# Optimization experiments

Hardware: AMD Instinct MI355X
Metric: run time of the kernel (lower is better)

## Reference

```python
import jax, jax.numpy as jnp
import numpy as np

D_K = 64

def setup_inputs() -> dict:
    key = jax.random.key(0)
    kq, kk, kv, km = jax.random.split(key, 4)
    B, H, S, D = 8, 8, 1024, D_K
    Q = jax.random.normal(kq, (B, H, S, D), dtype=jnp.float32)
    K = jax.random.normal(kk, (B, H, S, D), dtype=jnp.float32)
    V = jax.random.normal(kv, (B, H, S, D), dtype=jnp.float32)
    attention_masks = (jax.random.uniform(km, (B, 1, 1, S)) > 0.1).astype(jnp.float32)
    return {"Q": Q, "K": K, "V": V, "attention_masks": attention_masks}

def reference(Q, K, V, attention_masks):
    # scores = exp(QK^T / sqrt(d_k))  -- raw exp, NO max-subtraction (faithful to source)
    scale = 1.0 / np.sqrt(D_K).astype(np.float32)
    scores = jnp.exp(jnp.einsum('bhqd,bhkd->bhqk', Q, K) * scale)
    scores = scores * attention_masks  # multiplicative masking
    attention_scores = scores / (jnp.sum(scores, axis=-1, keepdims=True) + 1e-8)
    context = jnp.einsum('bhqk,bhkd->bhqd', attention_scores, V)
    return (context, attention_scores)
```

## Files before the change

kernel.cpp:

```cpp
#include <hip/hip_runtime.h>


typedef float    f32x4 __attribute__((ext_vector_type(4)));
typedef _Float16 f16x8 __attribute__((ext_vector_type(8)));
typedef _Float16 f16x4 __attribute__((ext_vector_type(4)));

#define MFMA32(A, B, C) __builtin_amdgcn_mfma_f32_16x16x32_f16((A), (B), (C), 0, 0, 0)
#define MFMA16(A, B, C) __builtin_amdgcn_mfma_f32_16x16x16f16((A), (B), (C), 0, 0, 0)

#define BHN 64
#define SEQ 1024
#define DIM 64

__device__ inline f16x8 cvt8(f32x4 a, f32x4 b) {
    f16x8 r;
    r[0] = (_Float16)a[0]; r[1] = (_Float16)a[1]; r[2] = (_Float16)a[2]; r[3] = (_Float16)a[3];
    r[4] = (_Float16)b[0]; r[5] = (_Float16)b[1]; r[6] = (_Float16)b[2]; r[7] = (_Float16)b[3];
    return r;
}

__global__ __launch_bounds__(256)
void cvt_kv(const float* __restrict__ K, const float* __restrict__ V,
            _Float16* __restrict__ Kh, _Float16* __restrict__ VTP)
{
    __shared__ _Float16 tile[128 * 65];
    const int bh = blockIdx.x >> 3;
    const int kc = blockIdx.x & 7;
    const int t  = threadIdx.x;
    const size_t base = ((size_t)bh * SEQ + (size_t)kc * 128) * DIM;

    for (int it = 0; it < 8; ++it) {
        int idx = it * 256 + t;
        int key = idx >> 4;
        int c4  = idx & 15;
        f32x4 kv = *(const f32x4*)(K + base + key * DIM + c4 * 4);
        f32x4 vv = *(const f32x4*)(V + base + key * DIM + c4 * 4);
        f16x4 kh4;
        kh4[0] = (_Float16)kv[0]; kh4[1] = (_Float16)kv[1];
        kh4[2] = (_Float16)kv[2]; kh4[3] = (_Float16)kv[3];
        *(f16x4*)(Kh + base + key * DIM + c4 * 4) = kh4;
        tile[key * 65 + c4 * 4 + 0] = (_Float16)vv[0];
        tile[key * 65 + c4 * 4 + 1] = (_Float16)vv[1];
        tile[key * 65 + c4 * 4 + 2] = (_Float16)vv[2];
        tile[key * 65 + c4 * 4 + 3] = (_Float16)vv[3];
    }
    __syncthreads();
    for (int it = 0; it < 8; ++it) {
        int flat = it * 256 + t;
        int ktl  = flat >> 8;
        int rem  = flat & 255;
        int l    = rem >> 2;
        int c    = rem & 3;
        f16x4 o;
        #pragma unroll
        for (int j = 0; j < 4; ++j)
            o[j] = tile[(ktl * 16 + ((l >> 4) << 2) + j) * 65 + c * 16 + (l & 15)];
        *(f16x4*)(VTP + (((size_t)bh * 64 + kc * 8 + ktl) * 64 + l) * 16 + c * 4) = o;
    }
}

template <bool PRECONV>
__global__ __launch_bounds__(256, 2)
void attn_main(const float* __restrict__ Q, const float* __restrict__ K,
               const float* __restrict__ V, const float* __restrict__ mask,
               const _Float16* __restrict__ Kh, const _Float16* __restrict__ VTP,
               float* __restrict__ ctx, float* __restrict__ scores)
{
    __shared__ _Float16 Et[32 * 1024];
    __shared__ float rs[4][2][16];

    const int bid = blockIdx.x;
    const int wg  = ((bid & 7) << 8) | (bid >> 3);
    const int bh  = wg >> 5;
    const int qb  = wg & 31;
    const int b   = bh >> 3;
    const int w    = threadIdx.x >> 6;
    const int lane = threadIdx.x & 63;
    const int col  = lane & 15;
    const int g    = lane >> 4;
    const int q0   = qb * 32;
    const int kb   = w * 256;
    const float scale = 0.125f;
    char* EtB = (char*)Et;

    f16x8 qf[2][2];
    {
        const float* qbase = Q + ((size_t)bh * SEQ + q0) * DIM;
        #pragma unroll
        for (int s = 0; s < 2; ++s)
            #pragma unroll
            for (int f = 0; f < 2; ++f) {
                const float* p = qbase + (s * 16 + col) * DIM + f * 32 + g * 8;
                qf[s][f] = cvt8(*(const f32x4*)p, *(const f32x4*)(p + 4));
            }
    }
    const float* mb = mask + (size_t)b * SEQ + kb;
    const _Float16* kbase = Kh + ((size_t)bh * SEQ + kb + col) * DIM + g * 8;
    const _Float16* vtpb  = VTP + (((size_t)bh * 64 + w * 16) * 64 + lane) * 16;

    f32x4 cacc[2][4];
    #pragma unroll
    for (int s = 0; s < 2; ++s)
        #pragma unroll
        for (int dt = 0; dt < 4; ++dt) cacc[s][dt] = (f32x4){0.f, 0.f, 0.f, 0.f};
    float rsum[2] = {0.f, 0.f};

    auto loadS = [&](int kt, f16x8& a, f16x8& c, f16x8& x, f16x8& y, f32x4& m) {
        if (PRECONV) {
            a = *(const f16x8*)(kbase + (size_t)kt * 16 * DIM);
            c = *(const f16x8*)(kbase + (size_t)kt * 16 * DIM + 32);
            x = *(const f16x8*)(vtpb + (size_t)kt * 64 * 16);
            y = *(const f16x8*)(vtpb + (size_t)kt * 64 * 16 + 8);
        } else {
            const float* kp = K + ((size_t)bh * SEQ + kb + kt * 16 + col) * DIM + g * 8;
            a = cvt8(*(const f32x4*)kp,        *(const f32x4*)(kp + 4));
            c = cvt8(*(const f32x4*)(kp + 32), *(const f32x4*)(kp + 36));
            #pragma unroll
            for (int e = 0; e < 8; ++e) {
                x[e] = (_Float16)V[((size_t)bh * SEQ + kb + kt * 16 + g * 4 + (e & 3)) * DIM + (e >> 2) * 16 + col];
                y[e] = (_Float16)V[((size_t)bh * SEQ + kb + kt * 16 + g * 4 + (e & 3)) * DIM + (2 + (e >> 2)) * 16 + col];
            }
        }
        m = *(const f32x4*)(mb + kt * 16 + g * 4);
    };

    auto body = [&](int kt, f16x8 k0, f16x8 k1, f16x8 va, f16x8 vb, f32x4 m4) {
        f16x4 pf[2];
        #pragma unroll
        for (int s = 0; s < 2; ++s) {
            f32x4 acc = {0.f, 0.f, 0.f, 0.f};
            acc = MFMA32(k0, qf[s][0], acc);
            acc = MFMA32(k1, qf[s][1], acc);
            const float e0 = __expf(acc[0] * scale) * m4[0];
            const float e1 = __expf(acc[1] * scale) * m4[1];
            const float e2 = __expf(acc[2] * scale) * m4[2];
            const float e3 = __expf(acc[3] * scale) * m4[3];
            rsum[s] += e0 + e1 + e2 + e3;
            f16x4 eh;
            eh[0] = (_Float16)e0; eh[1] = (_Float16)e1;
            eh[2] = (_Float16)e2; eh[3] = (_Float16)e3;
            pf[s] = eh;
            const int row = s * 16 + col;
            const int kg  = (w * 64 + kt * 4 + g) ^ ((row & 3) << 2);
            *(f16x4*)(EtB + row * 2048 + kg * 8) = eh;
        }
        f16x4 vt0 = __builtin_shufflevector(va, va, 0, 1, 2, 3);
        f16x4 vt1 = __builtin_shufflevector(va, va, 4, 5, 6, 7);
        f16x4 vt2 = __builtin_shufflevector(vb, vb, 0, 1, 2, 3);
        f16x4 vt3 = __builtin_shufflevector(vb, vb, 4, 5, 6, 7);
        cacc[0][0] = MFMA16(vt0, pf[0], cacc[0][0]);
        cacc[1][0] = MFMA16(vt0, pf[1], cacc[1][0]);
        cacc[0][1] = MFMA16(vt1, pf[0], cacc[0][1]);
        cacc[1][1] = MFMA16(vt1, pf[1], cacc[1][1]);
        cacc[0][2] = MFMA16(vt2, pf[0], cacc[0][2]);
        cacc[1][2] = MFMA16(vt2, pf[1], cacc[1][2]);
        cacc[0][3] = MFMA16(vt3, pf[0], cacc[0][3]);
        cacc[1][3] = MFMA16(vt3, pf[1], cacc[1][3]);
    };

    f16x8 k0A, k1A, vaA, vbA, k0B, k1B, vaB, vbB;
    f32x4 m4A, m4B;
    loadS(0, k0A, k1A, vaA, vbA, m4A);
    loadS(1, k0B, k1B, vaB, vbB, m4B);

    #pragma unroll 1
    for (int kt = 0; kt < 16; kt += 2) {
        f16x8 n0, n1, nx, ny;
        f32x4 nm;
        loadS((kt + 2) & 15, n0, n1, nx, ny, nm);
        body(kt, k0A, k1A, vaA, vbA, m4A);
        k0A = n0; k1A = n1; vaA = nx; vbA = ny; m4A = nm;

        loadS((kt + 3) & 15, n0, n1, nx, ny, nm);
        body(kt + 1, k0B, k1B, vaB, vbB, m4B);
        k0B = n0; k1B = n1; vaB = nx; vbB = ny; m4B = nm;
    }

    #pragma unroll
    for (int s = 0; s < 2; ++s) {
        float r = rsum[s];
        r += __shfl_xor(r, 16, 64);
        r += __shfl_xor(r, 32, 64);
        rsum[s] = r;
    }
    if (g == 0) {
        rs[w][0][col] = rsum[0];
        rs[w][1][col] = rsum[1];
    }
    __syncthreads();

    const int r0 = w * 8;
    float* srow = scores + ((size_t)bh * SEQ + q0) * SEQ;
    for (int j = 0; j < 8; ++j) {
        const int r  = r0 + j;
        const int si = r >> 4, ci = r & 15;
        const float invr = 1.0f / (rs[0][si][ci] + rs[1][si][ci] + rs[2][si][ci] + rs[3][si][ci] + 1e-8f);
        f16x4 ev[4];
        #pragma unroll
        for (int q = 0; q < 4; ++q) {
            const int kg = (q * 64 + lane) ^ ((r & 3) << 2);
            ev[q] = *(const f16x4*)(EtB + r * 2048 + kg * 8);
        }
        float* dst = srow + (size_t)r * SEQ + lane * 4;
        #pragma unroll
        for (int q = 0; q < 4; ++q) {
            f32x4 o;
            o[0] = (float)ev[q][0] * invr;
            o[1] = (float)ev[q][1] * invr;
            o[2] = (float)ev[q][2] * invr;
            o[3] = (float)ev[q][3] * invr;
            __builtin_nontemporal_store(o, (f32x4*)(dst + q * 256));
        }
    }

    __syncthreads();

    float* dumpf = (float*)Et;
    if (w != 0) {
        float* d = dumpf + (w - 1) * 2048;
        #pragma unroll
        for (int s = 0; s < 2; ++s)
            #pragma unroll
            for (int dt = 0; dt < 4; ++dt)
                #pragma unroll
                for (int i = 0; i < 4; ++i)
                    d[((s * 4 + dt) * 4 + i) * 64 + lane] = cacc[s][dt][i];
    }
    __syncthreads();
    if (w == 0) {
        #pragma unroll
        for (int s = 0; s < 2; ++s) {
            const float invs = 1.0f / (rs[0][s][col] + rs[1][s][col] + rs[2][s][col] + rs[3][s][col] + 1e-8f);
            #pragma unroll
            for (int dt = 0; dt < 4; ++dt) {
                f32x4 r = cacc[s][dt];
                #pragma unroll
                for (int ww = 0; ww < 3; ++ww) {
                    const float* d = dumpf + ww * 2048;
                    #pragma unroll
                    for (int i = 0; i < 4; ++i)
                        r[i] += d[((s * 4 + dt) * 4 + i) * 64 + lane];
                }
                r[0] *= invs; r[1] *= invs; r[2] *= invs; r[3] *= invs;
                *(f32x4*)(ctx + ((size_t)bh * SEQ + q0 + s * 16 + col) * DIM + dt * 16 + g * 4) = r;
            }
        }
    }
}

extern "C" void kernel_launch(void* const* d_in, const int* in_sizes, int n_in,
                              void* d_out, int out_size, void* d_ws, size_t ws_size,
                              hipStream_t stream)
{
    const float* Q    = (const float*)d_in[0];
    const float* K    = (const float*)d_in[1];
    const float* V    = (const float*)d_in[2];
    const float* mask = (const float*)d_in[3];
    float* ctx    = (float*)d_out;
    float* scores = ctx + (size_t)BHN * SEQ * DIM;

    const size_t elems = (size_t)BHN * SEQ * DIM;
    const size_t need  = elems * 2 * sizeof(_Float16);
    if (ws_size >= need) {
        _Float16* Kh  = (_Float16*)d_ws;
        _Float16* VTP = Kh + elems;
        cvt_kv<<<512, 256, 0, stream>>>(K, V, Kh, VTP);
        attn_main<true><<<2048, 256, 0, stream>>>(Q, K, V, mask, Kh, VTP, ctx, scores);
    } else {
        attn_main<false><<<2048, 256, 0, stream>>>(Q, K, V, mask, nullptr, nullptr, ctx, scores);
    }
}
```

Measured before the change: 93.83 us.

## Split attention into rowsum pass and streamed normalized score/PV pass

Adds a separate kernel that computes QK^T exponentials only to get per-row inverse sums. The main kernel then recomputes the scores already normalized and streams them to global memory in small double-buffered shared-memory chunks interleaved with the loop, instead of holding a full 32x1024 tile and writing it after a barrier. The intent is to overlap the large scores write with compute and cut shared-memory footprint. The cost is a second QK^T plus exp pass and an extra launch. The fallback path writes invp into the workspace without checking its size.

```diff
diff --git a/kernel.cpp b/kernel.cpp
--- a/kernel.cpp
+++ b/kernel.cpp
@@ -60,14 +60,90 @@
 }
 
 template <bool PRECONV>
+__global__ __launch_bounds__(256, 4)
+void rowsum_k(const float* __restrict__ Q, const float* __restrict__ K,
+              const float* __restrict__ mask, const _Float16* __restrict__ Kh,
+              float* __restrict__ invp)
+{
+    __shared__ float rs[4][4][16];
+    const int bid = blockIdx.x;
+    const int wg  = ((bid & 7) << 7) | (bid >> 3);
+    const int bh  = wg >> 4;
+    const int qb  = wg & 15;
+    const int b   = bh >> 3;
+    const int w    = threadIdx.x >> 6;
+    const int lane = threadIdx.x & 63;
+    const int col  = lane & 15;
+    const int g    = lane >> 4;
+    const int q0   = qb * 64;
+    const int kb   = w * 256;
+    const float scale = 0.125f;
+
+    f16x8 qf[4][2];
+    {
+        const float* qbase = Q + ((size_t)bh * SEQ + q0) * DIM;
+        #pragma unroll
+        for (int s = 0; s < 4; ++s)
+            #pragma unroll
+            for (int f = 0; f < 2; ++f) {
+                const float* p = qbase + (s * 16 + col) * DIM + f * 32 + g * 8;
+                qf[s][f] = cvt8(*(const f32x4*)p, *(const f32x4*)(p + 4));
+            }
+    }
+    const float* mb = mask + (size_t)b * SEQ + kb;
+
+    float rsum[4] = {0.f, 0.f, 0.f, 0.f};
+    #pragma unroll 1
+    for (int kt = 0; kt < 16; ++kt) {
+        f16x8 kf0, kf1;
+        if (PRECONV) {
+            const _Float16* kp = Kh + ((size_t)bh * SEQ + kb + kt * 16 + col) * DIM + g * 8;
+            kf0 = *(const f16x8*)kp;
+            kf1 = *(const f16x8*)(kp + 32);
+        } else {
+            const float* kp = K + ((size_t)bh * SEQ + kb + kt * 16 + col) * DIM + g * 8;
+            kf0 = cvt8(*(const f32x4*)kp,        *(const f32x4*)(kp + 4));
+            kf1 = cvt8(*(const f32x4*)(kp + 32), *(const f32x4*)(kp + 36));
+        }
+        f32x4 m4 = *(const f32x4*)(mb + kt * 16 + g * 4);
+        #pragma unroll
+        for (int s = 0; s < 4; ++s) {
+            f32x4 acc = {0.f, 0.f, 0.f, 0.f};
+            acc = MFMA32(kf0, qf[s][0], acc);
+            acc = MFMA32(kf1, qf[s][1], acc);
+            rsum[s] += __expf(acc[0] * scale) * m4[0] + __expf(acc[1] * scale) * m4[1]
+                     + __expf(acc[2] * scale) * m4[2] + __expf(acc[3] * scale) * m4[3];
+        }
+    }
+    #pragma unroll
+    for (int s = 0; s < 4; ++s) {
+        float r = rsum[s];
+        r += __shfl_xor(r, 16, 64);
+        r += __shfl_xor(r, 32, 64);
+        rsum[s] = r;
+    }
+    if (g == 0) {
+        #pragma unroll
+        for (int s = 0; s < 4; ++s) rs[w][s][col] = rsum[s];
+    }
+    __syncthreads();
+    if (w == 0) {
+        const int r = lane;
+        const float t = rs[0][r >> 4][r & 15] + rs[1][r >> 4][r & 15]
+                      + rs[2][r >> 4][r & 15] + rs[3][r >> 4][r & 15];
+        invp[(size_t)bh * SEQ + q0 + r] = 1.0f / (t + 1e-8f);
+    }
+}
+
+template <bool PRECONV>
 __global__ __launch_bounds__(256, 2)
-void attn_main(const float* __restrict__ Q, const float* __restrict__ K,
+void scorepv_k(const float* __restrict__ Q, const float* __restrict__ K,
                const float* __restrict__ V, const float* __restrict__ mask,
                const _Float16* __restrict__ Kh, const _Float16* __restrict__ VTP,
+               const float* __restrict__ invp,
                float* __restrict__ ctx, float* __restrict__ scores)
 {
-    __shared__ _Float16 Et[32 * 1024];
-    __shared__ float rs[4][2][16];
+    __shared__ _Float16 EC[4 * 2 * 32 * 64];
 
     const int bid = blockIdx.x;
     const int wg  = ((bid & 7) << 8) | (bid >> 3);
@@ -81,7 +157,7 @@
     const int q0   = qb * 32;
     const int kb   = w * 256;
     const float scale = 0.125f;
-    char* EtB = (char*)Et;
+    char* ECw = (char*)EC + w * 8192;
 
     f16x8 qf[2][2];
     {
@@ -94,16 +170,20 @@
                 qf[s][f] = cvt8(*(const f32x4*)p, *(const f32x4*)(p + 4));
             }
     }
+    float inv[2];
+    inv[0] = invp[(size_t)bh * SEQ + q0 + col];
+    inv[1] = invp[(size_t)bh * SEQ + q0 + 16 + col];
+
     const float* mb = mask + (size_t)b * SEQ + kb;
     const _Float16* kbase = Kh + ((size_t)bh * SEQ + kb + col) * DIM + g * 8;
     const _Float16* vtpb  = VTP + (((size_t)bh * 64 + w * 16) * 64 + lane) * 16;
+    float* srow = scores + ((size_t)bh * SEQ + q0) * SEQ + kb;
 
     f32x4 cacc[2][4];
     #pragma unroll
     for (int s = 0; s < 2; ++s)
         #pragma unroll
         for (int dt = 0; dt < 4; ++dt) cacc[s][dt] = (f32x4){0.f, 0.f, 0.f, 0.f};
-    float rsum[2] = {0.f, 0.f};
 
     auto loadS = [&](int kt, f16x8& a, f16x8& c, f16x8& x, f16x8& y, f32x4& m) {
         if (PRECONV) {
@@ -124,98 +204,75 @@
         m = *(const f32x4*)(mb + kt * 16 + g * 4);
     };
 
-    auto body = [&](int kt, f16x8 k0, f16x8 k1, f16x8 va, f16x8 vb, f32x4 m4) {
+    auto flushInstr = [&](int cf, int fb, int m) {
+        const int rm  = m * 4 + g;
+        const int gsw = (col ^ (rm & 15));
+        f16x4 ev = *(const f16x4*)(ECw + fb * 4096 + rm * 128 + gsw * 8);
+        f32x4 o;
+        o[0] = (float)ev[0]; o[1] = (float)ev[1];
+        o[2] = (float)ev[2]; o[3] = (float)ev[3];
+        __builtin_nontemporal_store(o, (f32x4*)(srow + (size_t)rm * SEQ + cf * 64 + col * 4));
+    };
+
+    f16x8 k0, k1, va, vb;
+    f32x4 m4;
+    loadS(0, k0, k1, va, vb, m4);
+
+    #pragma unroll 1
+    for (int kt = 0; kt < 16; ++kt) {
+        f16x8 n0, n1, nx, ny;
+        f32x4 nm;
+        loadS((kt + 1) & 15, n0, n1, nx, ny, nm);
+
+        if (kt >= 4) {
+            const int cf = (kt >> 2) - 1;
+            const int fb = cf & 1;
+            flushInstr(cf, fb, (kt & 3) * 2);
+            flushInstr(cf, fb, (kt & 3) * 2 + 1);
+        }
+
+        const int buf = (kt >> 2) & 1;
         f16x4 pf[2];
         #pragma unroll
         for (int s = 0; s < 2; ++s) {
             f32x4 acc = {0.f, 0.f, 0.f, 0.f};
             acc = MFMA32(k0, qf[s][0], acc);
             acc = MFMA32(k1, qf[s][1], acc);
-            const float e0 = __expf(acc[0] * scale) * m4[0];
-            const float e1 = __expf(acc[1] * scale) * m4[1];
-            const float e2 = __expf(acc[2] * scale) * m4[2];
-            const float e3 = __expf(acc[3] * scale) * m4[3];
-            rsum[s] += e0 + e1 + e2 + e3;
+            const float p0 = __expf(acc[0] * scale) * m4[0] * inv[s];
+            const float p1 = __expf(acc[1] * scale) * m4[1] * inv[s];
+            const float p2 = __expf(acc[2] * scale) * m4[2] * inv[s];
+            const float p3 = __expf(acc[3] * scale) * m4[3] * inv[s];
             f16x4 eh;
-            eh[0] = (_Float16)e0; eh[1] = (_Float16)e1;
-            eh[2] = (_Float16)e2; eh[3] = (_Float16)e3;
+            eh[0] = (_Float16)p0; eh[1] = (_Float16)p1;
+            eh[2] = (_Float16)p2; eh[3] = (_Float16)p3;
             pf[s] = eh;
             const int row = s * 16 + col;
-            const int kg  = (w * 64 + kt * 4 + g) ^ ((row & 3) << 2);
-            *(f16x4*)(EtB + row * 2048 + kg * 8) = eh;
-        }
-        f16x4 vt0 = __builtin_shufflevector(va, va, 0, 1, 2, 3);
-        f16x4 vt1 = __builtin_shufflevector(va, va, 4, 5, 6, 7);
-        f16x4 vt2 = __builtin_shufflevector(vb, vb, 0, 1, 2, 3);
-        f16x4 vt3 = __builtin_shufflevector(vb, vb, 4, 5, 6, 7);
-        cacc[0][0] = MFMA16(vt0, pf[0], cacc[0][0]);
-        cacc[1][0] = MFMA16(vt0, pf[1], cacc[1][0]);
-        cacc[0][1] = MFMA16(vt1, pf[0], cacc[0][1]);
-        cacc[1][1] = MFMA16(vt1, pf[1], cacc[1][1]);
-        cacc[0][2] = MFMA16(vt2, pf[0], cacc[0][2]);
-        cacc[1][2] = MFMA16(vt2, pf[1], cacc[1][2]);
-        cacc[0][3] = MFMA16(vt3, pf[0], cacc[0][3]);
-        cacc[1][3] = MFMA16(vt3, pf[1], cacc[1][3]);
-    };
-
-    f16x8 k0A, k1A, vaA, vbA, k0B, k1B, vaB, vbB;
-    f32x4 m4A, m4B;
-    loadS(0, k0A, k1A, vaA, vbA, m4A);
-    loadS(1, k0B, k1B, vaB, vbB, m4B);
-
-    #pragma unroll 1
-    for (int kt = 0; kt < 16; kt += 2) {
-        f16x8 n0, n1, nx, ny;
-        f32x4 nm;
-        loadS((kt + 2) & 15, n0, n1, nx, ny, nm);
-        body(kt, k0A, k1A, vaA, vbA, m4A);
-        k0A = n0; k1A = n1; vaA = nx; vbA = ny; m4A = nm;
-
-        loadS((kt + 3) & 15, n0, n1, nx, ny, nm);
-        body(kt + 1, k0B, k1B, vaB, vbB, m4B);
-        k0B = n0; k1B = n1; vaB = nx; vbB = ny; m4B = nm;
+            const int gg  = ((kt & 3) * 4 + g) ^ (row & 15);
+            *(f16x4*)(ECw + buf * 4096 + row * 128 + gg * 8) = eh;
+        }
+        {
+            f16x4 vt0 = __builtin_shufflevector(va, va, 0, 1, 2, 3);
+            f16x4 vt1 = __builtin_shufflevector(va, va, 4, 5, 6, 7);
+            f16x4 vt2 = __builtin_shufflevector(vb, vb, 0, 1, 2, 3);
+            f16x4 vt3 = __builtin_shufflevector(vb, vb, 4, 5, 6, 7);
+            cacc[0][0] = MFMA16(vt0, pf[0], cacc[0][0]);
+            cacc[1][0] = MFMA16(vt0, pf[1], cacc[1][0]);
+            cacc[0][1] = MFMA16(vt1, pf[0], cacc[0][1]);
+            cacc[1][1] = MFMA16(vt1, pf[1], cacc[1][1]);
+            cacc[0][2] = MFMA16(vt2, pf[0], cacc[0][2]);
+            cacc[1][2] = MFMA16(vt2, pf[1], cacc[1][2]);
+            cacc[0][3] = MFMA16(vt3, pf[0], cacc[0][3]);
+            cacc[1][3] = MFMA16(vt3, pf[1], cacc[1][3]);
+        }
+        k0 = n0; k1 = n1; va = nx; vb = ny; m4 = nm;
     }
 
     #pragma unroll
-    for (int s = 0; s < 2; ++s) {
-        float r = rsum[s];
-        r += __shfl_xor(r, 16, 64);
-        r += __shfl_xor(r, 32, 64);
-        rsum[s] = r;
-    }
-    if (g == 0) {
-        rs[w][0][col] = rsum[0];
-        rs[w][1][col] = rsum[1];
-    }
+    for (int m = 0; m < 8; ++m) flushInstr(3, 1, m);
+
     __syncthreads();
 
-    const int r0 = w * 8;
-    float* srow = scores + ((size_t)bh * SEQ + q0) * SEQ;
-    for (int j = 0; j < 8; ++j) {
-        const int r  = r0 + j;
-        const int si = r >> 4, ci = r & 15;
-        const float invr = 1.0f / (rs[0][si][ci] + rs[1][si][ci] + rs[2][si][ci] + rs[3][si][ci] + 1e-8f);
-        f16x4 ev[4];
-        #pragma unroll
-        for (int q = 0; q < 4; ++q) {
-            const int kg = (q * 64 + lane) ^ ((r & 3) << 2);
-            ev[q] = *(const f16x4*)(EtB + r * 2048 + kg * 8);
-        }
-        float* dst = srow + (size_t)r * SEQ + lane * 4;
-        #pragma unroll
-        for (int q = 0; q < 4; ++q) {
-            f32x4 o;
-            o[0] = (float)ev[q][0] * invr;
-            o[1] = (float)ev[q][1] * invr;
-            o[2] = (float)ev[q][2] * invr;
-            o[3] = (float)ev[q][3] * invr;
-            __builtin_nontemporal_store(o, (f32x4*)(dst + q * 256));
-        }
-    }
-
-    __syncthreads();
-
-    float* dumpf = (float*)Et;
+    float* dumpf = (float*)EC;
     if (w != 0) {
         float* d = dumpf + (w - 1) * 2048;
         #pragma unroll
@@ -229,8 +286,7 @@
     __syncthreads();
     if (w == 0) {
         #pragma unroll
-        for (int s = 0; s < 2; ++s) {
-            const float invs = 1.0f / (rs[0][s][col] + rs[1][s][col] + rs[2][s][col] + rs[3][s][col] + 1e-8f);
+        for (int s = 0; s < 2; ++s)
             #pragma unroll
             for (int dt = 0; dt < 4; ++dt) {
                 f32x4 r = cacc[s][dt];
@@ -241,10 +297,8 @@
                     for (int i = 0; i < 4; ++i)
                         r[i] += d[((s * 4 + dt) * 4 + i) * 64 + lane];
                 }
-                r[0] *= invs; r[1] *= invs; r[2] *= invs; r[3] *= invs;
                 *(f32x4*)(ctx + ((size_t)bh * SEQ + q0 + s * 16 + col) * DIM + dt * 16 + g * 4) = r;
             }
-        }
     }
 }
 
@@ -260,13 +314,19 @@
     float* scores = ctx + (size_t)BHN * SEQ * DIM;
 
     const size_t elems = (size_t)BHN * SEQ * DIM;
-    const size_t need  = elems * 2 * sizeof(_Float16);
+    const size_t inv_bytes = (size_t)BHN * SEQ * sizeof(float);
+    const size_t need = elems * 2 * sizeof(_Float16) + inv_bytes;
+
     if (ws_size >= need) {
-        _Float16* Kh  = (_Float16*)d_ws;
-        _Float16* VTP = Kh + elems;
+        _Float16* Kh   = (_Float16*)d_ws;
+        _Float16* VTP  = Kh + elems;
+        float*    invp = (float*)(VTP + elems);
         cvt_kv<<<512, 256, 0, stream>>>(K, V, Kh, VTP);
-        attn_main<true><<<2048, 256, 0, stream>>>(Q, K, V, mask, Kh, VTP, ctx, scores);
+        rowsum_k<true><<<1024, 256, 0, stream>>>(Q, K, mask, Kh, invp);
+        scorepv_k<true><<<2048, 256, 0, stream>>>(Q, K, V, mask, Kh, VTP, invp, ctx, scores);
     } else {
-        attn_main<false><<<2048, 256, 0, stream>>>(Q, K, V, mask, nullptr, nullptr, ctx, scores);
-    }
-}
+        float* invp = (float*)d_ws;
+        rowsum_k<false><<<1024, 256, 0, stream>>>(Q, K, mask, nullptr, invp);
+        scorepv_k<false><<<2048, 256, 0, stream>>>(Q, K, V, mask, nullptr, nullptr, invp, ctx, scores);
+    }
+}
```

New measurement: 102.7 us. +9.5%, slower.
